# Kernel optimization log

Measured on AMD Instinct MI355X. Metric: run time of the kernel, lower is better.

The kernel has to match this reference:

```python
import jax, jax.numpy as jnp
import numpy as np

N, C, A = 8192, 1000, 2048


def setup_inputs() -> dict:
    key = jax.random.key(0)
    k1, k2, k3, k4, k5, k6 = jax.random.split(key, 6)
    return {
        "fc": jax.random.normal(k1, (C, A), dtype=jnp.float32) * 0.02,
        "features_source": jax.random.normal(k2, (N, A), dtype=jnp.float32),
        "y_s": jax.random.normal(k3, (N, C), dtype=jnp.float32),
        "labels_source": jax.random.randint(k4, (N,), 0, C),
        "ratio": jnp.ones((1,), dtype=jnp.float32),
        "weights": jax.random.uniform(k5, (C,), dtype=jnp.float32, minval=0.5, maxval=1.5),
        "cv": jax.random.uniform(k6, (C, A), dtype=jnp.float32),
    }


def _metasaug_logits(fc, y_s, labels, cv, ratio):
    # sigma2[i,j] = ratio * sum_a (W[j,a] - W[y_i,a])^2 * cv[y_i,a]
    # expand the square -> three GEMM/reduction terms, avoiding the NxCxA tensor
    cv_y = cv[labels]            # (N, A)
    W_y = fc[labels]             # (N, A)
    term1 = cv_y @ (fc * fc).T                                   # (N, C)
    term2 = jnp.sum((W_y * W_y) * cv_y, axis=-1, keepdims=True)  # (N, 1)
    term3 = (W_y * cv_y) @ fc.T                                  # (N, C)
    sigma2 = ratio * (term1 + term2 - 2.0 * term3)
    return y_s + 0.5 * sigma2


def reference(fc, features_source, y_s, labels_source, ratio, weights, cv):
    # mode != 'update' path: augmented logits + class-weighted cross entropy
    aug_y = _metasaug_logits(fc, y_s, labels_source, cv, ratio)
    logp = jax.nn.log_softmax(aug_y, axis=-1)
    nll = -jnp.take_along_axis(logp, labels_source[:, None], axis=1)[:, 0]  # (N,)
    w = weights[labels_source]
    # torch weighted CE with mean reduction divides by sum of per-sample weights
    return jnp.sum(w * nll) / jnp.sum(w)
```

## Files before the change

### kernel.cpp

```cpp
#include <hip/hip_runtime.h>
#include <hip/hip_fp16.h>

#define N_SAMP 8192
#define C_CLS  1000
#define A_DIM  2048
#define KDIM   4096
#define CP     1024
#define ZSPLIT 8

typedef _Float16 half8 __attribute__((ext_vector_type(8)));
typedef _Float16 half4 __attribute__((ext_vector_type(4)));
typedef float    f32x4 __attribute__((ext_vector_type(4)));
typedef unsigned int u32x2 __attribute__((ext_vector_type(2)));

__global__ __launch_bounds__(256) void prep_kernel(const float* __restrict__ fc,
                                                   const float* __restrict__ cv,
                                                   unsigned char* __restrict__ Ab,
                                                   unsigned char* __restrict__ Bb) {
    int i4 = blockIdx.x * 256 + threadIdx.x;
    int c  = i4 >> 9;
    int k4 = i4 & 511;
    f32x4 f = {0.f, 0.f, 0.f, 0.f}, v = {0.f, 0.f, 0.f, 0.f};
    if (c < C_CLS) {
        size_t off = (size_t)c * (A_DIM / 4) + k4;
        f = ((const f32x4*)fc)[off];
        v = ((const f32x4*)cv)[off];
    }
    int alo = 0, ahi = 0, blo = 0, bhi = 0;
    alo = __builtin_amdgcn_cvt_pk_fp8_f32(v[0], v[1], alo, 0);
    alo = __builtin_amdgcn_cvt_pk_fp8_f32(v[2], v[3], alo, 1);
    ahi = __builtin_amdgcn_cvt_pk_fp8_f32(-32.f * f[0] * v[0], -32.f * f[1] * v[1], ahi, 0);
    ahi = __builtin_amdgcn_cvt_pk_fp8_f32(-32.f * f[2] * v[2], -32.f * f[3] * v[3], ahi, 1);
    blo = __builtin_amdgcn_cvt_pk_fp8_f32(256.f * f[0] * f[0], 256.f * f[1] * f[1], blo, 0);
    blo = __builtin_amdgcn_cvt_pk_fp8_f32(256.f * f[2] * f[2], 256.f * f[3] * f[3], blo, 1);
    bhi = __builtin_amdgcn_cvt_pk_fp8_f32(16.f * f[0], 16.f * f[1], bhi, 0);
    bhi = __builtin_amdgcn_cvt_pk_fp8_f32(16.f * f[2], 16.f * f[3], bhi, 1);
    size_t ro = (size_t)c * KDIM + k4 * 4;
    *(int*)(Ab + ro)         = alo;
    *(int*)(Ab + ro + A_DIM) = ahi;
    *(int*)(Bb + ro)         = blo;
    *(int*)(Bb + ro + A_DIM) = bhi;
}

template<int Z>
__global__ __launch_bounds__(256) void gemm_kernel(const unsigned char* __restrict__ A,
                                                   const unsigned char* __restrict__ B,
                                                   unsigned char* __restrict__ Spart) {
    constexpr int KS = KDIM / Z;
    constexpr int NT = KS / 64;
    __shared__ unsigned char As[2][128][64];
    __shared__ unsigned char Bs[2][64][64];

    const int z  = blockIdx.x;
    const int tj = blockIdx.y;
    const int tc = blockIdx.z;
    const int tid = threadIdx.x;
    const int lane = tid & 63;
    const int w  = tid >> 6;
    const int wr = w >> 1, wc = w & 1;
    const int k0 = z * KS;

    const size_t arow0 = (size_t)tc * 128;
    const size_t brow0 = (size_t)tj * 64;

#define STAGE(p, kcur)                                                                  \
    {                                                                                   \
        _Pragma("unroll")                                                               \
        for (int issue = 0; issue < 2; ++issue) {                                       \
            int t16 = issue * 256 + tid;                                                \
            int row = t16 >> 2, gp = t16 & 3;                                           \
            int gs  = gp ^ ((row >> 1) & 3);                                            \
            const unsigned char* ga = A + (arow0 + row) * KDIM + (kcur) + gs * 16;      \
            char* la = (char*)&As[p][0][0] + t16 * 16;                                  \
            __builtin_amdgcn_global_load_lds(                                           \
                (const __attribute__((address_space(1))) void*)ga,                      \
                (__attribute__((address_space(3))) void*)la, 16, 0, 0);                 \
        }                                                                               \
        {                                                                               \
            int row = tid >> 2, gp = tid & 3;                                           \
            int gs  = gp ^ ((row >> 1) & 3);                                            \
            const unsigned char* gb = B + (brow0 + row) * KDIM + (kcur) + gs * 16;      \
            char* lb = (char*)&Bs[p][0][0] + tid * 16;                                  \
            __builtin_amdgcn_global_load_lds(                                           \
                (const __attribute__((address_space(1))) void*)gb,                      \
                (__attribute__((address_space(3))) void*)lb, 16, 0, 0);                 \
        }                                                                               \
    }

    f32x4 acc[4][2] = {};
    const int r16 = lane & 15;
    const int g   = lane >> 4;

    STAGE(0, k0);
    __syncthreads();
    for (int t = 0; t < NT; ++t) {
        int cur = t & 1;
        if (t + 1 < NT) STAGE(cur ^ 1, k0 + (t + 1) * 64);
        #pragma unroll
        for (int kh = 0; kh < 2; kh++) {
            const int gidx = kh * 2 + (g >> 1);
            const int sub  = (g & 1) * 8;
            long af[4], bf[2];
            #pragma unroll
            for (int m = 0; m < 4; m++) {
                int row = wr * 64 + m * 16 + r16;
                af[m] = *(const long*)&As[cur][row][((gidx ^ ((row >> 1) & 3)) << 4) + sub];
            }
            #pragma unroll
            for (int n = 0; n < 2; n++) {
                int row = wc * 32 + n * 16 + r16;
                bf[n] = *(const long*)&Bs[cur][row][((gidx ^ ((row >> 1) & 3)) << 4) + sub];
            }
            #pragma unroll
            for (int m = 0; m < 4; m++)
                #pragma unroll
                for (int n = 0; n < 2; n++)
                    acc[m][n] = __builtin_amdgcn_mfma_f32_16x16x32_fp8_fp8(af[m], bf[n], acc[m][n], 0, 0, 0);
        }
        __syncthreads();
    }
#undef STAGE

    unsigned char* Sp = Spart + (size_t)z * CP * CP;
    int drow = (lane >> 4) * 4;
    int dcol = lane & 15;
    #pragma unroll
    for (int m = 0; m < 4; m++)
        #pragma unroll
        for (int n = 0; n < 2; n++)
            #pragma unroll
            for (int r = 0; r < 4; r++) {
                int pk = __builtin_amdgcn_cvt_pk_fp8_f32(acc[m][n][r], acc[m][n][r], 0, 0);
                Sp[(size_t)(tc * 128 + wr * 64 + m * 16 + drow + r) * CP
                   + tj * 64 + wc * 32 + n * 16 + dcol] = (unsigned char)(pk & 0xff);
            }
}

template<int Z>
__global__ __launch_bounds__(256) void ksum_kernel(const unsigned char* __restrict__ Spart,
                                                   _Float16* __restrict__ S) {
    size_t idx = (size_t)blockIdx.x * 256 + threadIdx.x;
    float a[8] = {};
    #pragma unroll
    for (int z = 0; z < Z; z++) {
        u32x2 v = *(const u32x2*)(Spart + (size_t)z * CP * CP + idx * 8);
        a[0] += __builtin_amdgcn_cvt_f32_fp8(v.x, 0);
        a[1] += __builtin_amdgcn_cvt_f32_fp8(v.x, 1);
        a[2] += __builtin_amdgcn_cvt_f32_fp8(v.x, 2);
        a[3] += __builtin_amdgcn_cvt_f32_fp8(v.x, 3);
        a[4] += __builtin_amdgcn_cvt_f32_fp8(v.y, 0);
        a[5] += __builtin_amdgcn_cvt_f32_fp8(v.y, 1);
        a[6] += __builtin_amdgcn_cvt_f32_fp8(v.y, 2);
        a[7] += __builtin_amdgcn_cvt_f32_fp8(v.y, 3);
    }
    half8 o;
    #pragma unroll
    for (int t = 0; t < 8; t++) o[t] = (_Float16)a[t];
    ((half8*)S)[idx] = o;
}

__global__ __launch_bounds__(256) void row_nll_kernel(const float* __restrict__ y_s,
                                                      const _Float16* __restrict__ S,
                                                      const int* __restrict__ labels,
                                                      const float* __restrict__ ratio,
                                                      const float* __restrict__ weights,
                                                      float* __restrict__ partial) {
    int lane = threadIdx.x & 63;
    int w = threadIdx.x >> 6;
    int i = blockIdx.x * 4 + w;
    int y = labels[i];
    float h = 0.5f * ratio[0] * (1.0f / 256.0f);
    const float*    ys_row = y_s + (size_t)i * C_CLS;
    const _Float16* s_row  = S   + (size_t)y * CP;

    float v[16];
    float m = -INFINITY;
    #pragma unroll
    for (int k = 0; k < 4; k++) {
        int j = lane * 4 + 256 * k;
        if (j < C_CLS) {
            f32x4 ys = *(const f32x4*)(ys_row + j);
            half4 sv = *(const half4*)(s_row + j);
            #pragma unroll
            for (int t = 0; t < 4; t++) {
                float val = ys[t] + h * (float)sv[t];
                v[k * 4 + t] = val;
                m = fmaxf(m, val);
            }
        } else {
            #pragma unroll
            for (int t = 0; t < 4; t++) v[k * 4 + t] = -INFINITY;
        }
    }
    #pragma unroll
    for (int off = 32; off; off >>= 1) m = fmaxf(m, __shfl_xor(m, off));
    float s = 0.f;
    #pragma unroll
    for (int k = 0; k < 16; k++) s += __expf(v[k] - m);
    #pragma unroll
    for (int off = 32; off; off >>= 1) s += __shfl_xor(s, off);

    __shared__ float swn[4], sww[4];
    if (lane == 0) {
        float target = ys_row[y] + h * (float)s_row[y];
        float wgt = weights[y];
        swn[w] = wgt * ((m + logf(s)) - target);
        sww[w] = wgt;
    }
    __syncthreads();
    if (threadIdx.x == 0) {
        partial[2 * blockIdx.x]     = swn[0] + swn[1] + swn[2] + swn[3];
        partial[2 * blockIdx.x + 1] = sww[0] + sww[1] + sww[2] + sww[3];
    }
}

#define NBLK_NLL (N_SAMP / 4)

__global__ __launch_bounds__(256) void finalize_kernel(const float* __restrict__ partial,
                                                       float* __restrict__ out) {
    float a = 0.f, b = 0.f;
    for (int i = threadIdx.x; i < NBLK_NLL; i += 256) {
        a += partial[2 * i];
        b += partial[2 * i + 1];
    }
    #pragma unroll
    for (int off = 32; off; off >>= 1) { a += __shfl_xor(a, off); b += __shfl_xor(b, off); }
    __shared__ float wa[4], wb[4];
    int w = threadIdx.x >> 6;
    if ((threadIdx.x & 63) == 0) { wa[w] = a; wb[w] = b; }
    __syncthreads();
    if (threadIdx.x == 0)
        out[0] = (wa[0] + wa[1] + wa[2] + wa[3]) / (wb[0] + wb[1] + wb[2] + wb[3]);
}

extern "C" void kernel_launch(void* const* d_in, const int* in_sizes, int n_in,
                              void* d_out, int out_size, void* d_ws, size_t ws_size,
                              hipStream_t stream) {
    const float* fc      = (const float*)d_in[0];
    const float* y_s     = (const float*)d_in[2];
    const int*   labels  = (const int*)d_in[3];
    const float* ratio   = (const float*)d_in[4];
    const float* weights = (const float*)d_in[5];
    const float* cv      = (const float*)d_in[6];

    char* ws = (char*)d_ws;
    unsigned char* Abuf  = (unsigned char*)ws;
    unsigned char* Bbuf  = (unsigned char*)(ws + (size_t)4 * 1024 * 1024);
    unsigned char* Spart = (unsigned char*)(ws + (size_t)8 * 1024 * 1024);
    _Float16*      S     = (_Float16*)(ws + (size_t)16 * 1024 * 1024);
    float*         part  = (float*)   (ws + (size_t)18 * 1024 * 1024);

    prep_kernel<<<(CP * A_DIM / 4) / 256, 256, 0, stream>>>(fc, cv, Abuf, Bbuf);
    gemm_kernel<ZSPLIT><<<dim3(ZSPLIT, 16, 8), 256, 0, stream>>>(Abuf, Bbuf, Spart);
    ksum_kernel<ZSPLIT><<<(CP * CP / 8) / 256, 256, 0, stream>>>(Spart, S);
    row_nll_kernel<<<NBLK_NLL, 256, 0, stream>>>(y_s, S, labels, ratio, weights, part);
    finalize_kernel<<<1, 256, 0, stream>>>(part, (float*)d_out);
}
```

Measured before the change: 38.34 us.

## Switch fp8 GEMM to 32x32x64 scaled MFMA with 128x128 tiles

Replaces the 16x16x32 fp8 MFMA with the gfx950 32x32x64 f8f6f4 scaled MFMA (unit scales) and enlarges the B tile from 64 to 128 rows, so each block computes a 128x128 output tile. The grid halves in the j dimension, each wave issues fewer, larger MFMAs per k-step, and LDS reads become 16-byte vector loads. This is meant to raise MFMA throughput and operand reuse, at the cost of more LDS per block, fewer blocks (512) to fill the GPU, and a different output lane layout that must match the 32x32 accumulator mapping.

After: 35.91 us, median of 2. 1.07x faster.

```diff
diff --git a/kernel.cpp b/kernel.cpp
--- a/kernel.cpp
+++ b/kernel.cpp
@@ -11,6 +11,9 @@
 typedef _Float16 half8 __attribute__((ext_vector_type(8)));
 typedef _Float16 half4 __attribute__((ext_vector_type(4)));
 typedef float    f32x4 __attribute__((ext_vector_type(4)));
+typedef float    f32x16 __attribute__((ext_vector_type(16)));
+typedef int      i32x4 __attribute__((ext_vector_type(4)));
+typedef int      i32x8 __attribute__((ext_vector_type(8)));
 typedef unsigned int u32x2 __attribute__((ext_vector_type(2)));
 
 __global__ __launch_bounds__(256) void prep_kernel(const float* __restrict__ fc,
@@ -49,7 +52,7 @@
     constexpr int KS = KDIM / Z;
     constexpr int NT = KS / 64;
     __shared__ unsigned char As[2][128][64];
-    __shared__ unsigned char Bs[2][64][64];
+    __shared__ unsigned char Bs[2][128][64];
 
     const int z  = blockIdx.x;
     const int tj = blockIdx.y;
@@ -61,7 +64,7 @@
     const int k0 = z * KS;
 
     const size_t arow0 = (size_t)tc * 128;
-    const size_t brow0 = (size_t)tj * 64;
+    const size_t brow0 = (size_t)tj * 128;
 
 #define STAGE(p, kcur)                                                                  \
     {                                                                                   \
@@ -71,68 +74,67 @@
             int row = t16 >> 2, gp = t16 & 3;                                           \
             int gs  = gp ^ ((row >> 1) & 3);                                            \
             const unsigned char* ga = A + (arow0 + row) * KDIM + (kcur) + gs * 16;      \
+            const unsigned char* gb = B + (brow0 + row) * KDIM + (kcur) + gs * 16;      \
             char* la = (char*)&As[p][0][0] + t16 * 16;                                  \
+            char* lb = (char*)&Bs[p][0][0] + t16 * 16;                                  \
             __builtin_amdgcn_global_load_lds(                                           \
                 (const __attribute__((address_space(1))) void*)ga,                      \
                 (__attribute__((address_space(3))) void*)la, 16, 0, 0);                 \
-        }                                                                               \
-        {                                                                               \
-            int row = tid >> 2, gp = tid & 3;                                           \
-            int gs  = gp ^ ((row >> 1) & 3);                                            \
-            const unsigned char* gb = B + (brow0 + row) * KDIM + (kcur) + gs * 16;      \
-            char* lb = (char*)&Bs[p][0][0] + tid * 16;                                  \
             __builtin_amdgcn_global_load_lds(                                           \
                 (const __attribute__((address_space(1))) void*)gb,                      \
                 (__attribute__((address_space(3))) void*)lb, 16, 0, 0);                 \
         }                                                                               \
     }
 
-    f32x4 acc[4][2] = {};
-    const int r16 = lane & 15;
-    const int g   = lane >> 4;
+    f32x16 acc[2][2] = {};
+    const int r32   = lane & 31;
+    const int khalf = lane >> 5;
+    const int g0 = khalf * 2, g1 = khalf * 2 + 1;
 
     STAGE(0, k0);
     __syncthreads();
     for (int t = 0; t < NT; ++t) {
         int cur = t & 1;
         if (t + 1 < NT) STAGE(cur ^ 1, k0 + (t + 1) * 64);
-        #pragma unroll
-        for (int kh = 0; kh < 2; kh++) {
-            const int gidx = kh * 2 + (g >> 1);
-            const int sub  = (g & 1) * 8;
-            long af[4], bf[2];
-            #pragma unroll
-            for (int m = 0; m < 4; m++) {
-                int row = wr * 64 + m * 16 + r16;
-                af[m] = *(const long*)&As[cur][row][((gidx ^ ((row >> 1) & 3)) << 4) + sub];
-            }
-            #pragma unroll
-            for (int n = 0; n < 2; n++) {
-                int row = wc * 32 + n * 16 + r16;
-                bf[n] = *(const long*)&Bs[cur][row][((gidx ^ ((row >> 1) & 3)) << 4) + sub];
-            }
-            #pragma unroll
-            for (int m = 0; m < 4; m++)
-                #pragma unroll
-                for (int n = 0; n < 2; n++)
-                    acc[m][n] = __builtin_amdgcn_mfma_f32_16x16x32_fp8_fp8(af[m], bf[n], acc[m][n], 0, 0, 0);
+        i32x8 af[2], bf[2];
+        #pragma unroll
+        for (int m = 0; m < 2; m++) {
+            int row = wr * 64 + m * 32 + r32;
+            int sw  = (row >> 1) & 3;
+            i32x4 lo = *(const i32x4*)&As[cur][row][(g0 ^ sw) << 4];
+            i32x4 hi = *(const i32x4*)&As[cur][row][(g1 ^ sw) << 4];
+            af[m] = __builtin_shufflevector(lo, hi, 0, 1, 2, 3, 4, 5, 6, 7);
         }
+        #pragma unroll
+        for (int n = 0; n < 2; n++) {
+            int row = wc * 64 + n * 32 + r32;
+            int sw  = (row >> 1) & 3;
+            i32x4 lo = *(const i32x4*)&Bs[cur][row][(g0 ^ sw) << 4];
+            i32x4 hi = *(const i32x4*)&Bs[cur][row][(g1 ^ sw) << 4];
+            bf[n] = __builtin_shufflevector(lo, hi, 0, 1, 2, 3, 4, 5, 6, 7);
+        }
+        #pragma unroll
+        for (int m = 0; m < 2; m++)
+            #pragma unroll
+            for (int n = 0; n < 2; n++)
+                acc[m][n] = __builtin_amdgcn_mfma_scale_f32_32x32x64_f8f6f4(
+                    af[m], bf[n], acc[m][n], 0 , 0 ,
+                    0, 127 , 0, 127 );
         __syncthreads();
     }
 #undef STAGE
 
     unsigned char* Sp = Spart + (size_t)z * CP * CP;
-    int drow = (lane >> 4) * 4;
-    int dcol = lane & 15;
-    #pragma unroll
-    for (int m = 0; m < 4; m++)
+    #pragma unroll
+    for (int m = 0; m < 2; m++)
         #pragma unroll
         for (int n = 0; n < 2; n++)
             #pragma unroll
-            for (int r = 0; r < 4; r++) {
+            for (int r = 0; r < 16; r++) {
+                int orow = (r & 3) + 8 * (r >> 2) + 4 * khalf;
                 int pk = __builtin_amdgcn_cvt_pk_fp8_f32(acc[m][n][r], acc[m][n][r], 0, 0);
-                Sp[(size_t)(tc * 128 + wr * 64 + m * 16 + drow + r) * CP
-                   + tj * 64 + wc * 32 + n * 16 + dcol] = (unsigned char)(pk & 0xff);
+                Sp[(size_t)(tc * 128 + wr * 64 + m * 32 + orow) * CP
+                   + tj * 128 + wc * 64 + n * 32 + r32] = (unsigned char)(pk & 0xff);
             }
 }
 
@@ -251,7 +253,7 @@
     float*         part  = (float*)   (ws + (size_t)18 * 1024 * 1024);
 
     prep_kernel<<<(CP * A_DIM / 4) / 256, 256, 0, stream>>>(fc, cv, Abuf, Bbuf);
-    gemm_kernel<ZSPLIT><<<dim3(ZSPLIT, 16, 8), 256, 0, stream>>>(Abuf, Bbuf, Spart);
+    gemm_kernel<ZSPLIT><<<dim3(ZSPLIT, 8, 8), 256, 0, stream>>>(Abuf, Bbuf, Spart);
     ksum_kernel<ZSPLIT><<<(CP * CP / 8) / 256, 256, 0, stream>>>(Spart, S);
     row_nll_kernel<<<NBLK_NLL, 256, 0, stream>>>(y_s, S, labels, ratio, weights, part);
     finalize_kernel<<<1, 256, 0, stream>>>(part, (float*)d_out);
```
